# Optimization experiments

Measured on AMD Instinct MI355X. Metric: run time of the kernel, lower is better.

## Reference

```python
import math
import jax, jax.numpy as jnp
import numpy as np

DIM = 512
STYLE_DIM = 512
WS = 8
RES = 64
HEADS = 16
SHIFT = WS // 2
B = 8
EPS = 1e-5


def _rel_pos_index(ws):
    # Faithful replica of the (non-standard) index construction in the source.
    coords = np.stack(np.meshgrid(np.arange(ws), np.arange(ws), indexing='ij')).reshape(2, -1)
    rc = (coords[:, :, None] - coords[:, None, :]).transpose(1, 2, 0).astype(np.int64)
    rc[:, :, 0] += ws - 1
    rc[:, :, 1] += ws - 1
    rc[:, :, 0] += 2 * ws - 1
    return jnp.asarray(rc.sum(-1))  # (ws*ws, ws*ws)


def _attn_mask2(res, ws):
    shift = ws // 2
    m = np.zeros((res, res), dtype=np.float32)
    cnt = 0
    for hs in [slice(0, -ws), slice(-ws, -shift), slice(-shift, None)]:
        for wsl in [slice(0, -ws), slice(-ws, -shift), slice(-shift, None)]:
            m[hs, wsl] = cnt
            cnt += 1
    mw = m.reshape(res // ws, ws, res // ws, ws).transpose(0, 2, 1, 3).reshape(-1, ws * ws)
    am = mw[:, None, :] - mw[:, :, None]  # (nW, N, N)
    return jnp.asarray(np.where(am != 0, -100.0, 0.0).astype(np.float32))


_RPI = _rel_pos_index(WS)
_MASK2 = _attn_mask2(RES, WS)


def _win_part(x, ws):
    Bc, H, W, C = x.shape
    x = x.reshape(Bc, H // ws, ws, W // ws, ws, C).transpose(0, 1, 3, 2, 4, 5)
    return x.reshape(-1, ws * ws, C)


def _win_rev(x, ws, H, W):
    nH, nW = H // ws, W // ws
    C = x.shape[-1]
    x = x.reshape(-1, nH, nW, ws, ws, C).transpose(0, 1, 3, 2, 4, 5)
    return x.reshape(-1, H, W, C)


def _adain(x, style, w, b):
    # x: (B, N, C); InstanceNorm1d over the token dim N per channel (biased var, no affine).
    scale = 1.0 / math.sqrt(w.shape[1])
    s = style @ (w * scale).T + b  # (B, 2C)
    C = x.shape[-1]
    gamma, beta = s[:, :C], s[:, C:]
    mean = x.mean(axis=1, keepdims=True)
    var = x.var(axis=1, keepdims=True)
    xn = (x - mean) / jnp.sqrt(var + EPS)
    return gamma[:, None, :] * xn + beta[:, None, :]


def _window_attn(q, k, v, ws, heads, rpb, rpi, mask):
    # q/k/v: (B, H, W, C)
    C = q.shape[-1]
    hd = C // heads
    qk_scale = hd ** -0.5
    qw = _win_part(q, ws)  # (Bw, N, C)
    kw = _win_part(k, ws)
    vw = _win_part(v, ws)
    Bw, N, _ = qw.shape
    qw = qw.reshape(Bw, N, heads, hd).transpose(0, 2, 1, 3)
    kw = kw.reshape(Bw, N, heads, hd).transpose(0, 2, 1, 3)
    vw = vw.reshape(Bw, N, heads, hd).transpose(0, 2, 1, 3)
    attn = jnp.einsum('bhnd,bhmd->bhnm', qw, kw) * qk_scale
    bias = rpb[rpi.reshape(-1)].reshape(N, N, heads).transpose(2, 0, 1)  # (h, N, N)
    attn = attn + bias[None]
    if mask is not None:
        nW = mask.shape[0]
        attn = attn.reshape(Bw // nW, nW, heads, N, N) + mask[None, :, None]
        attn = attn.reshape(Bw, heads, N, N)
    attn = jax.nn.softmax(attn, axis=-1)
    out = jnp.einsum('bhnm,bhmd->bhnd', attn, vw)
    return out.transpose(0, 2, 1, 3).reshape(Bw, N, C)


def _forward(x, style, ada1_w, ada1_b, qkv_w, qkv_b, rpb1, rpb2,
             proj_w, proj_b, ada2_w, ada2_b, mlp_w1, mlp_b1, mlp_w2, mlp_b2):
    H = W = RES
    Bc, N, C = x.shape
    shortcut = x
    xn = _adain(x, style, ada1_w, ada1_b)
    qkv = xn @ qkv_w.T + qkv_b  # (B, N, 3C)
    qkv = qkv.reshape(Bc, N, 3, C).transpose(2, 0, 1, 3).reshape(3, Bc, H, W, C)
    qkv1 = qkv[..., : C // 2]
    qkv2 = qkv[..., C // 2:]
    qkv2 = jnp.roll(qkv2, shift=(-SHIFT, -SHIFT), axis=(2, 3))
    x1 = _window_attn(qkv1[0], qkv1[1], qkv1[2], WS, HEADS // 2, rpb1, _RPI, None)
    x2 = _window_attn(qkv2[0], qkv2[1], qkv2[2], WS, HEADS // 2, rpb2, _RPI, _MASK2)
    x1 = _win_rev(x1, WS, H, W)
    x2 = _win_rev(x2, WS, H, W)
    x2 = jnp.roll(x2, shift=(SHIFT, SHIFT), axis=(1, 2))
    out = jnp.concatenate([x1, x2], axis=-1).reshape(Bc, N, C)
    out = out @ proj_w.T + proj_b
    out = shortcut + out
    xn2 = _adain(out, style, ada2_w, ada2_b)
    h = xn2 @ mlp_w1.T + mlp_b1
    h = jax.nn.gelu(h, approximate=False)  # erf-based gelu matches source
    h = h @ mlp_w2.T + mlp_b2
    return out + h


def setup_inputs() -> dict:
    key = jax.random.key(0)
    ks = jax.random.split(key, 16)
    rn = lambda k, shp, s: jax.random.normal(k, shp, dtype=jnp.float32) * s
    return {
        'x': rn(ks[0], (B, RES * RES, DIM), 1.0),
        'style': rn(ks[1], (B, STYLE_DIM), 1.0),
        'ada1_w': rn(ks[2], (2 * DIM, STYLE_DIM), 1.0),
        'ada1_b': rn(ks[3], (2 * DIM,), 0.02),
        'qkv_w': rn(ks[4], (3 * DIM, DIM), 0.02),
        'qkv_b': rn(ks[5], (3 * DIM,), 0.02),
        'rpb1': rn(ks[6], ((2 * WS - 1) ** 2, HEADS // 2), 0.02),
        'rpb2': rn(ks[7], ((2 * WS - 1) ** 2, HEADS // 2), 0.02),
        'proj_w': rn(ks[8], (DIM, DIM), 0.02),
        'proj_b': rn(ks[9], (DIM,), 0.02),
        'ada2_w': rn(ks[10], (2 * DIM, STYLE_DIM), 1.0),
        'ada2_b': rn(ks[11], (2 * DIM,), 0.02),
        'mlp_w1': rn(ks[12], (4 * DIM, DIM), 0.02),
        'mlp_b1': rn(ks[13], (4 * DIM,), 0.02),
        'mlp_w2': rn(ks[14], (DIM, 4 * DIM), 0.02),
        'mlp_b2': rn(ks[15], (DIM,), 0.02),
    }


def reference(x, style, ada1_w, ada1_b, qkv_w, qkv_b, rpb1, rpb2,
              proj_w, proj_b, ada2_w, ada2_b, mlp_w1, mlp_b1, mlp_w2, mlp_b2):
    return _forward(x, style, ada1_w, ada1_b, qkv_w, qkv_b, rpb1, rpb2,
                    proj_w, proj_b, ada2_w, ada2_b, mlp_w1, mlp_b1, mlp_w2, mlp_b2)
```

## Files before the change

### kernel.cpp

```cpp
#include <hip/hip_runtime.h>
#include <math.h>

typedef __attribute__((ext_vector_type(8))) short short8;
typedef __attribute__((ext_vector_type(4))) float f32x4;
typedef unsigned short ushort_t;

__device__ __forceinline__ float bf2f(ushort_t u) {
    return __uint_as_float(((unsigned int)u) << 16);
}
__device__ __forceinline__ ushort_t f2bf(float f) {
    unsigned int u = __float_as_uint(f);
    unsigned int r = u + 0x7fffu + ((u >> 16) & 1u);
    return (ushort_t)(r >> 16);
}

__device__ __forceinline__ void async_cp16(const void* g, void* l) {
    __builtin_amdgcn_global_load_lds((const __attribute__((address_space(1))) void*)g,
                                     (__attribute__((address_space(3))) void*)l, 16, 0, 0);
}

__device__ __forceinline__ float fast_gelu(float v) {
    float u2 = 2.0f * v * (0.7978845608028654f + 0.0356774081f * v * v);
    float e = __expf(u2);
    float r = 1.0f / (e + 1.0f);
    return v - v * r;
}

__global__ __launch_bounds__(256) void conv_zero(
        const float* __restrict__ qkv_w, ushort_t* __restrict__ qkv_wb,
        const float* __restrict__ proj_w, ushort_t* __restrict__ proj_wb,
        const float* __restrict__ w1, ushort_t* __restrict__ w1b,
        const float* __restrict__ w2, ushort_t* __restrict__ w2b,
        float* __restrict__ psum2, float* __restrict__ psq2) {
    int i = blockIdx.x * 256 + threadIdx.x;
    if (i < 786432) {
        qkv_wb[i] = f2bf(qkv_w[i]);
    } else if (i < 1048576) {
        int j = i - 786432; proj_wb[j] = f2bf(proj_w[j]);
    } else if (i < 2097152) {
        int j = i - 1048576; w1b[j] = f2bf(w1[j]);
    } else if (i < 3145728) {
        int j = i - 2097152; w2b[j] = f2bf(w2[j]);
    } else {
        int j = i - 3145728;
        psum2[j] = 0.f; psq2[j] = 0.f;
    }
}

__global__ __launch_bounds__(256) void style_kernel(const float* __restrict__ style,
        const float* __restrict__ w1, const float* __restrict__ b1,
        const float* __restrict__ w2, const float* __restrict__ b2,
        float* __restrict__ s1, float* __restrict__ s2) {
    int t = blockIdx.x * 256 + threadIdx.x;
    int which = t >> 13;
    int idx = t & 8191;
    int b = idx >> 10, j = idx & 1023;
    const float* w = which ? w2 : w1;
    const float* bb = which ? b2 : b1;
    const float* st = style + b * 512;
    const float* wr = w + (size_t)j * 512;
    float acc = 0.f;
    for (int k = 0; k < 512; ++k) acc += st[k] * wr[k];
    float v = acc * 0.04419417382415922f + bb[j];
    (which ? s2 : s1)[idx] = v;
}

__global__ __launch_bounds__(512) void stats_part(const float* __restrict__ x,
        float* __restrict__ psum, float* __restrict__ psq) {
    int b = blockIdx.x >> 5;
    int ch = blockIdx.x & 31;
    int c = threadIdx.x;
    const float* p = x + ((size_t)b * 4096 + (size_t)ch * 128) * 512 + c;
    float s = 0.f, q = 0.f;
    for (int t = 0; t < 128; ++t) {
        float v = p[(size_t)t * 512];
        s += v; q += v * v;
    }
    psum[(size_t)blockIdx.x * 512 + c] = s;
    psq [(size_t)blockIdx.x * 512 + c] = q;
}

__global__ __launch_bounds__(256) void stats_fin(const float* __restrict__ psum,
        const float* __restrict__ psq, float* __restrict__ mean, float* __restrict__ rstd) {
    int i = blockIdx.x * 256 + threadIdx.x;
    int b = i >> 9, c = i & 511;
    float s = 0.f, q = 0.f;
    for (int ch = 0; ch < 32; ++ch) {
        s += psum[(size_t)(b * 32 + ch) * 512 + c];
        q += psq [(size_t)(b * 32 + ch) * 512 + c];
    }
    float m = s * (1.f / 4096.f);
    float v = q * (1.f / 4096.f) - m * m;
    mean[i] = m;
    rstd[i] = rsqrtf(v + 1e-5f);
}

__global__ __launch_bounds__(256) void stats_fin2(const float* __restrict__ psum2,
        const float* __restrict__ psq2, float* __restrict__ mean, float* __restrict__ rstd) {
    int i = blockIdx.x * 256 + threadIdx.x;
    float m = psum2[i] * (1.f / 4096.f);
    float v = psq2[i] * (1.f / 4096.f) - m * m;
    mean[i] = m;
    rstd[i] = rsqrtf(v + 1e-5f);
}

__global__ __launch_bounds__(256) void adain_kernel(const float* __restrict__ x,
        const float* __restrict__ s, const float* __restrict__ mean,
        const float* __restrict__ rstd, ushort_t* __restrict__ xn) {
    size_t i4 = (size_t)blockIdx.x * 256 + threadIdx.x;
    size_t e = i4 * 4;
    int b = (int)(e >> 21);
    int c = (int)(e & 511);
    float4 xv = *(const float4*)(x + e);
    float vals[4] = {xv.x, xv.y, xv.z, xv.w};
    ushort_t o[4];
#pragma unroll
    for (int j = 0; j < 4; ++j) {
        int cc = c + j;
        float g  = s[b * 1024 + cc];
        float be = s[b * 1024 + 512 + cc];
        float mn = mean[b * 512 + cc];
        float rs = rstd[b * 512 + cc];
        o[j] = f2bf(g * (vals[j] - mn) * rs + be);
    }
    unsigned long long packed = (unsigned long long)o[0] |
        ((unsigned long long)o[1] << 16) | ((unsigned long long)o[2] << 32) |
        ((unsigned long long)o[3] << 48);
    *(unsigned long long*)(xn + e) = packed;
}

template<int EPI>
__global__ __launch_bounds__(512, 2) void gemm256(
        const ushort_t* __restrict__ A, const ushort_t* __restrict__ Bw,
        const float* __restrict__ bias, const float* __restrict__ resid,
        float* __restrict__ outf, ushort_t* __restrict__ outh,
        float* __restrict__ psum2, float* __restrict__ psq2,
        int N, int K, int gridN, int ntiles, int lnt) {
    __shared__ ushort_t lds[65536];
    const int tid  = threadIdx.x;
    const int lane = tid & 63;
    const int wave = tid >> 6;
    const int wm = wave >> 2, wn = wave & 3;
    const int lm = lane & 15;
    const int kg = lane >> 4;
    const int nt = 1 << lnt;
    const int tpb = ntiles >> 8;

    const int orig = blockIdx.x;
    const int wgid = (orig & 7) * 32 + (orig >> 3);

    unsigned int lo0 = lm * 128 + ((kg * 16) ^ ((lm & 7) << 4));
    unsigned int lo1 = lo0 ^ 64;
    unsigned int vA0 = wm * 16384 + lo0;
    unsigned int vA1 = wm * 16384 + lo1;
    unsigned int vB0 = 65536 + (wn >> 1) * 16384 + (wn & 1) * 8192 + lo0;
    unsigned int vB1 = 65536 + (wn >> 1) * 16384 + (wn & 1) * 8192 + lo1;
    const char* ldsc = (const char*)lds;

    int off[2][2];
#pragma unroll
    for (int rnd = 0; rnd < 2; ++rnd) {
        int chunk = tid + rnd * 512;
        int row = chunk >> 3;
        int g = chunk & 7;
        int gsw = g ^ (row & 7);
#pragma unroll
        for (int h = 0; h < 2; ++h)
            off[h][rnd] = (h * 128 + row) * K + gsw * 8;
    }

    f32x4 acc[8][4];
#pragma unroll
    for (int m = 0; m < 8; ++m)
#pragma unroll
        for (int n = 0; n < 4; ++n)
#pragma unroll
            for (int r = 0; r < 4; ++r) acc[m][n][r] = 0.f;

    auto stage = [&](const ushort_t* __restrict__ mat, long bcur, long bnxt,
                     int dslot, int h, int tt, int isB) {
        long mb = (tt < nt) ? bcur : bnxt;
        int kt = tt & (nt - 1);
        const ushort_t* base = mat + mb + (kt << 6);
        ushort_t* dst = (ushort_t*)lds + isB * 32768 + dslot * 16384 + h * 8192 + tid * 8;
#pragma unroll
        for (int rnd = 0; rnd < 2; ++rnd)
            async_cp16(base + off[h][rnd], dst + rnd * 4096);
    };

    int tcur = wgid;
    int bm = tcur / gridN, bn = tcur - bm * gridN;
    long Am = (long)bm * 256 * K;
    long Bn = (long)bn * 256 * K;

    stage(A,  Am, Am, 0, 0, 0, 0); stage(A,  Am, Am, 0, 1, 0, 0);
    stage(Bw, Bn, Bn, 0, 0, 0, 1); stage(Bw, Bn, Bn, 0, 1, 0, 1);
    stage(Bw, Bn, Bn, 1, 0, 1, 1); stage(Bw, Bn, Bn, 1, 1, 1, 1);
    asm volatile("s_waitcnt vmcnt(4)" ::: "memory");
    __builtin_amdgcn_sched_barrier(0);
    __builtin_amdgcn_s_barrier();

    for (int ti = 0; ti < tpb; ++ti) {
        int tnxt = (ti + 1 < tpb) ? tcur + 256 : tcur;
        int bm2 = tnxt / gridN, bn2 = tnxt - bm2 * gridN;
        long Am2 = (long)bm2 * 256 * K;
        long Bn2 = (long)bn2 * 256 * K;

#pragma unroll 2
        for (int t = 0; t < nt; ++t) {
            const int c = t & 1;
            short8 bfr[4][2];
#pragma unroll
            for (int q = 0; q < 4; ++q) {
                short8 af[2][2];
#pragma unroll
                for (int mq = 0; mq < 2; ++mq) {
                    af[mq][0] = *(const short8*)(ldsc + vA0 + (q * 4096 + mq * 2048));
                    af[mq][1] = *(const short8*)(ldsc + vA1 + (q * 4096 + mq * 2048));
                }
                if (q == 0) {
#pragma unroll
                    for (int n = 0; n < 4; ++n) {
                        bfr[n][0] = *(const short8*)(ldsc + vB0 + n * 2048);
                        bfr[n][1] = *(const short8*)(ldsc + vB1 + n * 2048);
                    }
                }
                if      (q == 0) stage(A,  Am, Am2, c ^ 1, 0, t + 1, 0);
                else if (q == 1) stage(A,  Am, Am2, c ^ 1, 1, t + 1, 0);
                else if (q == 2) stage(Bw, Bn, Bn2, c,     0, t + 2, 1);
                else             stage(Bw, Bn, Bn2, c,     1, t + 2, 1);

                __builtin_amdgcn_s_barrier();
                asm volatile("s_waitcnt lgkmcnt(0)" ::: "memory");
                __builtin_amdgcn_sched_barrier(0);
                __builtin_amdgcn_s_setprio(1);
#pragma unroll
                for (int mq = 0; mq < 2; ++mq)
#pragma unroll
                    for (int n = 0; n < 4; ++n)
#pragma unroll
                        for (int ks = 0; ks < 2; ++ks)
                            acc[q * 2 + mq][n] = __builtin_amdgcn_mfma_f32_16x16x32_bf16(
                                af[mq][ks], bfr[n][ks], acc[q * 2 + mq][n], 0, 0, 0);
                __builtin_amdgcn_s_setprio(0);
                if (q == 3) {
                    asm volatile("s_waitcnt vmcnt(4)" ::: "memory");
                    __builtin_amdgcn_sched_barrier(0);
                }
                __builtin_amdgcn_s_barrier();
            }
            vA0 ^= 32768u; vA1 ^= 32768u; vB0 ^= 32768u; vB1 ^= 32768u;
        }

        const long tile_m = (long)bm * 256;
        const long tile_n = (long)bn * 256;
        float csum[4], csq[4];
        if (EPI == 1) {
#pragma unroll
            for (int n = 0; n < 4; ++n) { csum[n] = 0.f; csq[n] = 0.f; }
        }
#pragma unroll
        for (int m = 0; m < 8; ++m) {
            long row0 = tile_m + wm * 128 + m * 16 + kg * 4;
#pragma unroll
            for (int n = 0; n < 4; ++n) {
                long col = tile_n + wn * 64 + n * 16 + lm;
                float bb = bias[col];
#pragma unroll
                for (int r = 0; r < 4; ++r) {
                    long o = (row0 + r) * (long)N + col;
                    float v = acc[m][n][r] + bb;
                    if (EPI == 0) {
                        outh[o] = f2bf(v);
                    } else if (EPI == 1) {
                        float w = v + resid[o];
                        outf[o] = w;
                        csum[n] += w; csq[n] += w * w;
                    } else if (EPI == 2) {
                        outh[o] = f2bf(fast_gelu(v));
                    } else {
                        outf[o] += v;
                    }
                    acc[m][n][r] = 0.f;
                }
            }
        }
        if (EPI == 1) {
            int b = (int)(tile_m >> 12);
#pragma unroll
            for (int n = 0; n < 4; ++n) {
                int col = (int)(tile_n + wn * 64 + n * 16 + lm);
                atomicAdd(&psum2[b * 512 + col], csum[n]);
                atomicAdd(&psq2 [b * 512 + col], csq[n]);
            }
        }

        tcur = tnxt; bm = bm2; bn = bn2; Am = Am2; Bn = Bn2;
    }
}

__global__ __launch_bounds__(64) void attn_kernel(const ushort_t* __restrict__ qkv,
        const float* __restrict__ rpb1, const float* __restrict__ rpb2,
        ushort_t* __restrict__ attno) {
    __shared__ float klds[64][36];
    __shared__ float vlds[64][36];
    int bid = blockIdx.x;
    int branch = bid >> 12;
    int w_idx  = (bid >> 3) & 511;
    int head   = bid & 7;
    int b = w_idx >> 6, win = w_idx & 63;
    int wh = win >> 3, ww = win & 7;
    int lane = threadIdx.x;
    int ti = lane >> 3, tj = lane & 7;
    int hh = wh * 8 + ti;
    int wp = ww * 8 + tj;
    int hs = branch ? ((hh + 4) & 63) : hh;
    int wsp = branch ? ((wp + 4) & 63) : wp;
    int n = hs * 64 + wsp;
    int c0 = branch * 256 + head * 32;
    const ushort_t* rowp = qkv + (size_t)(b * 4096 + n) * 1536;

    float q[32];
#pragma unroll
    for (int v8 = 0; v8 < 4; ++v8) {
        short8 t = *(const short8*)(rowp + c0 + v8 * 8);
#pragma unroll
        for (int i = 0; i < 8; ++i) q[v8 * 8 + i] = bf2f((ushort_t)t[i]);
    }
#pragma unroll
    for (int v8 = 0; v8 < 4; ++v8) {
        short8 tk = *(const short8*)(rowp + 512  + c0 + v8 * 8);
        short8 tv = *(const short8*)(rowp + 1024 + c0 + v8 * 8);
#pragma unroll
        for (int i = 0; i < 8; ++i) {
            klds[lane][v8 * 8 + i] = bf2f((ushort_t)tk[i]);
            vlds[lane][v8 * 8 + i] = bf2f((ushort_t)tv[i]);
        }
    }
    __syncthreads();

    const float* rpb = branch ? rpb2 : rpb1;
    int code_i = 0;
    if (branch) {
        int gh = (hh < 56) ? 0 : (hh < 60 ? 1 : 2);
        int gw = (wp < 56) ? 0 : (wp < 60 ? 1 : 2);
        code_i = gh * 3 + gw;
    }

    float s[64];
    float mx = -1e30f;
#pragma unroll
    for (int j = 0; j < 64; ++j) {
        int rj = j >> 3, cj = j & 7;
        const float4* kr4 = (const float4*)&klds[j][0];
        float4 k0 = kr4[0], k1 = kr4[1], k2 = kr4[2], k3 = kr4[3];
        float4 k4 = kr4[4], k5 = kr4[5], k6 = kr4[6], k7 = kr4[7];
        float acc =
            q[0]*k0.x + q[1]*k0.y + q[2]*k0.z + q[3]*k0.w +
            q[4]*k1.x + q[5]*k1.y + q[6]*k1.z + q[7]*k1.w +
            q[8]*k2.x + q[9]*k2.y + q[10]*k2.z + q[11]*k2.w +
            q[12]*k3.x + q[13]*k3.y + q[14]*k3.z + q[15]*k3.w +
            q[16]*k4.x + q[17]*k4.y + q[18]*k4.z + q[19]*k4.w +
            q[20]*k5.x + q[21]*k5.y + q[22]*k5.z + q[23]*k5.w +
            q[24]*k6.x + q[25]*k6.y + q[26]*k6.z + q[27]*k6.w +
            q[28]*k7.x + q[29]*k7.y + q[30]*k7.z + q[31]*k7.w;
        float sc = acc * 0.17677669529663687f + rpb[((ti - rj) + (tj - cj) + 29) * 8 + head];
        if (branch) {
            int hj = wh * 8 + rj, wj = ww * 8 + cj;
            int gh = (hj < 56) ? 0 : (hj < 60 ? 1 : 2);
            int gw = (wj < 56) ? 0 : (wj < 60 ? 1 : 2);
            if (gh * 3 + gw != code_i) sc -= 100.f;
        }
        s[j] = sc;
        mx = fmaxf(mx, sc);
    }
    float sum = 0.f;
#pragma unroll
    for (int j = 0; j < 64; ++j) { float e = __expf(s[j] - mx); s[j] = e; sum += e; }
    float inv = 1.f / sum;
    float o[32];
#pragma unroll
    for (int d = 0; d < 32; ++d) o[d] = 0.f;
#pragma unroll
    for (int j = 0; j < 64; ++j) {
        float p = s[j] * inv;
        const float4* vr4 = (const float4*)&vlds[j][0];
#pragma unroll
        for (int d4 = 0; d4 < 8; ++d4) {
            float4 vv = vr4[d4];
            o[d4 * 4 + 0] += p * vv.x;
            o[d4 * 4 + 1] += p * vv.y;
            o[d4 * 4 + 2] += p * vv.z;
            o[d4 * 4 + 3] += p * vv.w;
        }
    }
    ushort_t* op = attno + (size_t)(b * 4096 + n) * 512 + c0;
#pragma unroll
    for (int v8 = 0; v8 < 4; ++v8) {
        short8 t;
#pragma unroll
        for (int i = 0; i < 8; ++i) t[i] = (short)f2bf(o[v8 * 8 + i]);
        *(short8*)(op + v8 * 8) = t;
    }
}

extern "C" void kernel_launch(void* const* d_in, const int* in_sizes, int n_in,
                              void* d_out, int out_size, void* d_ws, size_t ws_size,
                              hipStream_t stream) {
    const float* x      = (const float*)d_in[0];
    const float* style  = (const float*)d_in[1];
    const float* ada1_w = (const float*)d_in[2];
    const float* ada1_b = (const float*)d_in[3];
    const float* qkv_w  = (const float*)d_in[4];
    const float* qkv_b  = (const float*)d_in[5];
    const float* rpb1   = (const float*)d_in[6];
    const float* rpb2   = (const float*)d_in[7];
    const float* proj_w = (const float*)d_in[8];
    const float* proj_b = (const float*)d_in[9];
    const float* ada2_w = (const float*)d_in[10];
    const float* ada2_b = (const float*)d_in[11];
    const float* mlp_w1 = (const float*)d_in[12];
    const float* mlp_b1 = (const float*)d_in[13];
    const float* mlp_w2 = (const float*)d_in[14];
    const float* mlp_b2 = (const float*)d_in[15];
    float* outf = (float*)d_out;

    char* W = (char*)d_ws;
    ushort_t* qkvb    = (ushort_t*)(W);
    ushort_t* attno   = (ushort_t*)(W + 100663296);
    ushort_t* hbuf    = (ushort_t*)(W);
    ushort_t* xn      = (ushort_t*)(W + 134217728);
    ushort_t* qkv_wb  = (ushort_t*)(W + 167772160);
    ushort_t* proj_wb = (ushort_t*)(W + 167772160 + 1572864);
    ushort_t* w1b     = (ushort_t*)(W + 167772160 + 2097152);
    ushort_t* w2b     = (ushort_t*)(W + 167772160 + 4194304);
    float* freg  = (float*)(W + 167772160 + 6291456);
    float* s1    = freg;
    float* s2    = freg + 8192;
    float* mean1 = freg + 16384;
    float* rstd1 = freg + 20480;
    float* mean2 = freg + 24576;
    float* rstd2 = freg + 28672;
    float* psum  = freg + 32768;
    float* psq   = freg + 163840;
    float* psum2 = freg + 294912;
    float* psq2  = freg + 303104;

    conv_zero<<<12320, 256, 0, stream>>>(qkv_w, qkv_wb, proj_w, proj_wb,
                                         mlp_w1, w1b, mlp_w2, w2b, psum2, psq2);

    style_kernel<<<64, 256, 0, stream>>>(style, ada1_w, ada1_b, ada2_w, ada2_b, s1, s2);

    stats_part<<<256, 512, 0, stream>>>(x, psum, psq);
    stats_fin<<<16, 256, 0, stream>>>(psum, psq, mean1, rstd1);
    adain_kernel<<<16384, 256, 0, stream>>>(x, s1, mean1, rstd1, xn);

    gemm256<0><<<256, 512, 0, stream>>>(xn, qkv_wb, qkv_b, nullptr, nullptr, qkvb,
                                        nullptr, nullptr, 1536, 512, 6, 768, 3);

    attn_kernel<<<8192, 64, 0, stream>>>(qkvb, rpb1, rpb2, attno);

    gemm256<1><<<256, 512, 0, stream>>>(attno, proj_wb, proj_b, x, outf, nullptr,
                                        psum2, psq2, 512, 512, 2, 256, 3);

    stats_fin2<<<16, 256, 0, stream>>>(psum2, psq2, mean2, rstd2);
    adain_kernel<<<16384, 256, 0, stream>>>(outf, s2, mean2, rstd2, xn);

    gemm256<2><<<256, 512, 0, stream>>>(xn, w1b, mlp_b1, nullptr, nullptr, hbuf,
                                        nullptr, nullptr, 2048, 512, 8, 1024, 3);
    gemm256<3><<<256, 512, 0, stream>>>(hbuf, w2b, mlp_b2, nullptr, outf, nullptr,
                                        nullptr, nullptr, 512, 2048, 2, 256, 5);
}
```

Baseline: 507.7 us.

## Rewrite window attention with bf16 MFMA and precomputed bias/mask tables

Replaces the scalar fp32 per-thread window attention with a wave-per-(window,head) kernel that computes QK^T and PV using bf16 16x16x32 MFMA instructions, staging V transposed and P in LDS. Relative-position bias and the shifted-window mask are folded into precomputed per-head float tables, built in the existing conversion kernel, so the per-element index and mask logic disappears from the hot loop. Softmax probabilities are rounded to bf16 before the PV product, which adds some precision loss. The tables add a small amount of extra setup work and global reads.

```diff
diff --git a/kernel.cpp b/kernel.cpp
--- a/kernel.cpp
+++ b/kernel.cpp
@@ -4,6 +4,7 @@
 typedef __attribute__((ext_vector_type(8))) short short8;
 typedef __attribute__((ext_vector_type(4))) float f32x4;
 typedef unsigned short ushort_t;
+typedef unsigned long long ull_t;
 
 __device__ __forceinline__ float bf2f(ushort_t u) {
     return __uint_as_float(((unsigned int)u) << 16);
@@ -12,6 +13,11 @@
     unsigned int u = __float_as_uint(f);
     unsigned int r = u + 0x7fffu + ((u >> 16) & 1u);
     return (ushort_t)(r >> 16);
+}
+__device__ __forceinline__ unsigned cvt_pk_bf16(float lo, float hi) {
+    unsigned r;
+    asm volatile("v_cvt_pk_bf16_f32 %0, %1, %2" : "=v"(r) : "v"(lo), "v"(hi));
+    return r;
 }
 
 __device__ __forceinline__ void async_cp16(const void* g, void* l) {
@@ -31,7 +37,9 @@
         const float* __restrict__ proj_w, ushort_t* __restrict__ proj_wb,
         const float* __restrict__ w1, ushort_t* __restrict__ w1b,
         const float* __restrict__ w2, ushort_t* __restrict__ w2b,
-        float* __restrict__ psum2, float* __restrict__ psq2) {
+        float* __restrict__ psum2, float* __restrict__ psq2,
+        const float* __restrict__ rpb1, const float* __restrict__ rpb2,
+        float* __restrict__ tbl0, float* __restrict__ tbl1) {
     int i = blockIdx.x * 256 + threadIdx.x;
     if (i < 786432) {
         qkv_wb[i] = f2bf(qkv_w[i]);
@@ -41,9 +49,31 @@
         int j = i - 1048576; w1b[j] = f2bf(w1[j]);
     } else if (i < 3145728) {
         int j = i - 2097152; w2b[j] = f2bf(w2[j]);
-    } else {
+    } else if (i < 3153920) {
         int j = i - 3145728;
         psum2[j] = 0.f; psq2[j] = 0.f;
+    } else {
+        int t = i - 3153920;
+        if (t < 32768) {
+            int h = t >> 12, ij = t & 4095;
+            int qi = ij >> 6, kj = ij & 63;
+            int idx = ((qi >> 3) - (kj >> 3)) + ((qi & 7) - (kj & 7)) + 29;
+            tbl0[t] = rpb1[idx * 8 + h];
+        } else {
+            int u = t - 32768;
+            int ij = u & 4095;
+            int cls = (u >> 12) & 3;
+            int h = u >> 14;
+            int qi = ij >> 6, kj = ij & 63;
+            int idx = ((qi >> 3) - (kj >> 3)) + ((qi & 7) - (kj & 7)) + 29;
+            float v = rpb2[idx * 8 + h];
+            int gh_i = (cls & 2) ? (((qi >> 3) < 4) ? 1 : 2) : 0;
+            int gw_i = (cls & 1) ? (((qi & 7) < 4) ? 1 : 2) : 0;
+            int gh_j = (cls & 2) ? (((kj >> 3) < 4) ? 1 : 2) : 0;
+            int gw_j = (cls & 1) ? (((kj & 7) < 4) ? 1 : 2) : 0;
+            if (gh_i * 3 + gw_i != gh_j * 3 + gw_j) v -= 100.f;
+            tbl1[u] = v;
+        }
     }
 }
 
@@ -123,10 +153,9 @@
         float rs = rstd[b * 512 + cc];
         o[j] = f2bf(g * (vals[j] - mn) * rs + be);
     }
-    unsigned long long packed = (unsigned long long)o[0] |
-        ((unsigned long long)o[1] << 16) | ((unsigned long long)o[2] << 32) |
-        ((unsigned long long)o[3] << 48);
-    *(unsigned long long*)(xn + e) = packed;
+    ull_t packed = (ull_t)o[0] |
+        ((ull_t)o[1] << 16) | ((ull_t)o[2] << 32) | ((ull_t)o[3] << 48);
+    *(ull_t*)(xn + e) = packed;
 }
 
 template<int EPI>
@@ -299,108 +328,171 @@
     }
 }
 
-__global__ __launch_bounds__(64) void attn_kernel(const ushort_t* __restrict__ qkv,
-        const float* __restrict__ rpb1, const float* __restrict__ rpb2,
+__global__ __launch_bounds__(256) void attn_mfma(const ushort_t* __restrict__ qkv,
+        const float* __restrict__ tbl0, const float* __restrict__ tbl1,
         ushort_t* __restrict__ attno) {
-    __shared__ float klds[64][36];
-    __shared__ float vlds[64][36];
-    int bid = blockIdx.x;
-    int branch = bid >> 12;
-    int w_idx  = (bid >> 3) & 511;
-    int head   = bid & 7;
-    int b = w_idx >> 6, win = w_idx & 63;
-    int wh = win >> 3, ww = win & 7;
-    int lane = threadIdx.x;
-    int ti = lane >> 3, tj = lane & 7;
-    int hh = wh * 8 + ti;
-    int wp = ww * 8 + tj;
-    int hs = branch ? ((hh + 4) & 63) : hh;
-    int wsp = branch ? ((wp + 4) & 63) : wp;
-    int n = hs * 64 + wsp;
-    int c0 = branch * 256 + head * 32;
-    const ushort_t* rowp = qkv + (size_t)(b * 4096 + n) * 1536;
-
-    float q[32];
-#pragma unroll
-    for (int v8 = 0; v8 < 4; ++v8) {
-        short8 t = *(const short8*)(rowp + c0 + v8 * 8);
-#pragma unroll
-        for (int i = 0; i < 8; ++i) q[v8 * 8 + i] = bf2f((ushort_t)t[i]);
-    }
-#pragma unroll
-    for (int v8 = 0; v8 < 4; ++v8) {
-        short8 tk = *(const short8*)(rowp + 512  + c0 + v8 * 8);
-        short8 tv = *(const short8*)(rowp + 1024 + c0 + v8 * 8);
-#pragma unroll
-        for (int i = 0; i < 8; ++i) {
-            klds[lane][v8 * 8 + i] = bf2f((ushort_t)tk[i]);
-            vlds[lane][v8 * 8 + i] = bf2f((ushort_t)tv[i]);
-        }
-    }
-    __syncthreads();
-
-    const float* rpb = branch ? rpb2 : rpb1;
-    int code_i = 0;
-    if (branch) {
-        int gh = (hh < 56) ? 0 : (hh < 60 ? 1 : 2);
-        int gw = (wp < 56) ? 0 : (wp < 60 ? 1 : 2);
-        code_i = gh * 3 + gw;
-    }
-
-    float s[64];
-    float mx = -1e30f;
-#pragma unroll
-    for (int j = 0; j < 64; ++j) {
-        int rj = j >> 3, cj = j & 7;
-        const float4* kr4 = (const float4*)&klds[j][0];
-        float4 k0 = kr4[0], k1 = kr4[1], k2 = kr4[2], k3 = kr4[3];
-        float4 k4 = kr4[4], k5 = kr4[5], k6 = kr4[6], k7 = kr4[7];
-        float acc =
-            q[0]*k0.x + q[1]*k0.y + q[2]*k0.z + q[3]*k0.w +
-            q[4]*k1.x + q[5]*k1.y + q[6]*k1.z + q[7]*k1.w +
-            q[8]*k2.x + q[9]*k2.y + q[10]*k2.z + q[11]*k2.w +
-            q[12]*k3.x + q[13]*k3.y + q[14]*k3.z + q[15]*k3.w +
-            q[16]*k4.x + q[17]*k4.y + q[18]*k4.z + q[19]*k4.w +
-            q[20]*k5.x + q[21]*k5.y + q[22]*k5.z + q[23]*k5.w +
-            q[24]*k6.x + q[25]*k6.y + q[26]*k6.z + q[27]*k6.w +
-            q[28]*k7.x + q[29]*k7.y + q[30]*k7.z + q[31]*k7.w;
-        float sc = acc * 0.17677669529663687f + rpb[((ti - rj) + (tj - cj) + 29) * 8 + head];
-        if (branch) {
-            int hj = wh * 8 + rj, wj = ww * 8 + cj;
-            int gh = (hj < 56) ? 0 : (hj < 60 ? 1 : 2);
-            int gw = (wj < 56) ? 0 : (wj < 60 ? 1 : 2);
-            if (gh * 3 + gw != code_i) sc -= 100.f;
-        }
-        s[j] = sc;
-        mx = fmaxf(mx, sc);
-    }
-    float sum = 0.f;
-#pragma unroll
-    for (int j = 0; j < 64; ++j) { float e = __expf(s[j] - mx); s[j] = e; sum += e; }
-    float inv = 1.f / sum;
-    float o[32];
-#pragma unroll
-    for (int d = 0; d < 32; ++d) o[d] = 0.f;
-#pragma unroll
-    for (int j = 0; j < 64; ++j) {
-        float p = s[j] * inv;
-        const float4* vr4 = (const float4*)&vlds[j][0];
-#pragma unroll
-        for (int d4 = 0; d4 < 8; ++d4) {
-            float4 vv = vr4[d4];
-            o[d4 * 4 + 0] += p * vv.x;
-            o[d4 * 4 + 1] += p * vv.y;
-            o[d4 * 4 + 2] += p * vv.z;
-            o[d4 * 4 + 3] += p * vv.w;
-        }
-    }
-    ushort_t* op = attno + (size_t)(b * 4096 + n) * 512 + c0;
-#pragma unroll
-    for (int v8 = 0; v8 < 4; ++v8) {
-        short8 t;
-#pragma unroll
-        for (int i = 0; i < 8; ++i) t[i] = (short)f2bf(o[v8 * 8 + i]);
-        *(short8*)(op + v8 * 8) = t;
+    __shared__ ushort_t lds[27648];
+    const int tid = threadIdx.x;
+    const int lane = tid & 63;
+    const int wave = tid >> 6;
+    const int job = blockIdx.x * 4 + wave;
+    const int branch = job >> 12;
+    const int w_idx  = (job >> 3) & 511;
+    const int head   = job & 7;
+    const int b = w_idx >> 6, win = w_idx & 63;
+    const int wh = win >> 3, ww = win & 7;
+    const int c0 = branch * 256 + head * 32;
+    const int i_lo = lane & 15;
+    const int kg = lane >> 4;
+
+    ushort_t* Vt = lds + wave * 6912;
+    ushort_t* P  = lds + wave * 6912 + 2304;
+
+    auto tokof = [&](int p) {
+        int hh = wh * 8 + (p >> 3), wp = ww * 8 + (p & 7);
+        if (branch) { hh = (hh + 4) & 63; wp = (wp + 4) & 63; }
+        return b * 4096 + hh * 64 + wp;
+    };
+
+    {
+        const ushort_t* vp = qkv + (size_t)tokof(lane) * 1536 + 1024 + c0;
+        short8 v0 = *(const short8*)(vp);
+        short8 v1 = *(const short8*)(vp + 8);
+        short8 v2 = *(const short8*)(vp + 16);
+        short8 v3 = *(const short8*)(vp + 24);
+#pragma unroll
+        for (int e = 0; e < 8; ++e) {
+            Vt[(e     ) * 72 + lane] = (ushort_t)v0[e];
+            Vt[(e +  8) * 72 + lane] = (ushort_t)v1[e];
+            Vt[(e + 16) * 72 + lane] = (ushort_t)v2[e];
+            Vt[(e + 24) * 72 + lane] = (ushort_t)v3[e];
+        }
+    }
+
+    short8 kf[4], qf[4];
+#pragma unroll
+    for (int m = 0; m < 4; ++m) {
+        size_t rowb = (size_t)tokof(m * 16 + i_lo) * 1536;
+        kf[m] = *(const short8*)(qkv + rowb + 512 + c0 + kg * 8);
+        qf[m] = *(const short8*)(qkv + rowb + c0 + kg * 8);
+    }
+
+    f32x4 s[4][4];
+#pragma unroll
+    for (int mj = 0; mj < 4; ++mj)
+#pragma unroll
+        for (int ni = 0; ni < 4; ++ni)
+#pragma unroll
+            for (int r = 0; r < 4; ++r) s[mj][ni][r] = 0.f;
+#pragma unroll
+    for (int mj = 0; mj < 4; ++mj)
+#pragma unroll
+        for (int ni = 0; ni < 4; ++ni)
+            s[mj][ni] = __builtin_amdgcn_mfma_f32_16x16x32_bf16(kf[mj], qf[ni], s[mj][ni], 0, 0, 0);
+
+    const float* tb;
+    if (branch == 0) {
+        tb = tbl0 + head * 4096;
+    } else {
+        int cls = ((wh == 7) ? 2 : 0) | ((ww == 7) ? 1 : 0);
+        tb = tbl1 + (head * 4 + cls) * 4096;
+    }
+#pragma unroll
+    for (int ni = 0; ni < 4; ++ni) {
+        int i = ni * 16 + i_lo;
+#pragma unroll
+        for (int mj = 0; mj < 4; ++mj) {
+            float4 bv = *(const float4*)(tb + i * 64 + mj * 16 + kg * 4);
+            s[mj][ni][0] = s[mj][ni][0] * 0.17677669529663687f + bv.x;
+            s[mj][ni][1] = s[mj][ni][1] * 0.17677669529663687f + bv.y;
+            s[mj][ni][2] = s[mj][ni][2] * 0.17677669529663687f + bv.z;
+            s[mj][ni][3] = s[mj][ni][3] * 0.17677669529663687f + bv.w;
+        }
+    }
+
+    float mx[4], rs[4];
+#pragma unroll
+    for (int ni = 0; ni < 4; ++ni) {
+        float m = -1e30f;
+#pragma unroll
+        for (int mj = 0; mj < 4; ++mj)
+#pragma unroll
+            for (int r = 0; r < 4; ++r) m = fmaxf(m, s[mj][ni][r]);
+        m = fmaxf(m, __shfl_xor(m, 16));
+        m = fmaxf(m, __shfl_xor(m, 32));
+        mx[ni] = m;
+    }
+#pragma unroll
+    for (int ni = 0; ni < 4; ++ni) {
+        float sum = 0.f;
+#pragma unroll
+        for (int mj = 0; mj < 4; ++mj)
+#pragma unroll
+            for (int r = 0; r < 4; ++r) {
+                float e = __expf(s[mj][ni][r] - mx[ni]);
+                s[mj][ni][r] = e;
+                sum += e;
+            }
+        sum += __shfl_xor(sum, 16);
+        sum += __shfl_xor(sum, 32);
+        rs[ni] = sum;
+    }
+
+#pragma unroll
+    for (int ni = 0; ni < 4; ++ni) {
+        int i = ni * 16 + i_lo;
+#pragma unroll
+        for (int mj = 0; mj < 4; ++mj) {
+            unsigned w0 = cvt_pk_bf16(s[mj][ni][0], s[mj][ni][1]);
+            unsigned w1 = cvt_pk_bf16(s[mj][ni][2], s[mj][ni][3]);
+            ull_t w = (ull_t)w0 | ((ull_t)w1 << 32);
+            *(ull_t*)&P[i * 72 + mj * 16 + kg * 4] = w;
+        }
+    }
+    asm volatile("s_waitcnt lgkmcnt(0)" ::: "memory");
+    __builtin_amdgcn_sched_barrier(0);
+
+    short8 va[2][2];
+    short8 pb[4][2];
+#pragma unroll
+    for (int md = 0; md < 2; ++md)
+#pragma unroll
+        for (int ks = 0; ks < 2; ++ks)
+            va[md][ks] = *(const short8*)&Vt[(md * 16 + i_lo) * 72 + ks * 32 + kg * 8];
+#pragma unroll
+    for (int ni = 0; ni < 4; ++ni)
+#pragma unroll
+        for (int ks = 0; ks < 2; ++ks)
+            pb[ni][ks] = *(const short8*)&P[(ni * 16 + i_lo) * 72 + ks * 32 + kg * 8];
+
+    f32x4 o[2][4];
+#pragma unroll
+    for (int md = 0; md < 2; ++md)
+#pragma unroll
+        for (int ni = 0; ni < 4; ++ni)
+#pragma unroll
+            for (int r = 0; r < 4; ++r) o[md][ni][r] = 0.f;
+#pragma unroll
+    for (int md = 0; md < 2; ++md)
+#pragma unroll
+        for (int ni = 0; ni < 4; ++ni)
+#pragma unroll
+            for (int ks = 0; ks < 2; ++ks)
+                o[md][ni] = __builtin_amdgcn_mfma_f32_16x16x32_bf16(va[md][ks], pb[ni][ks], o[md][ni], 0, 0, 0);
+
+#pragma unroll
+    for (int ni = 0; ni < 4; ++ni) {
+        float inv = 1.f / rs[ni];
+        ushort_t* op = attno + (size_t)tokof(ni * 16 + i_lo) * 512 + c0;
+#pragma unroll
+        for (int md = 0; md < 2; ++md) {
+            ushort_t h0 = f2bf(o[md][ni][0] * inv);
+            ushort_t h1 = f2bf(o[md][ni][1] * inv);
+            ushort_t h2 = f2bf(o[md][ni][2] * inv);
+            ushort_t h3 = f2bf(o[md][ni][3] * inv);
+            ull_t w = (ull_t)h0 | ((ull_t)h1 << 16) | ((ull_t)h2 << 32) | ((ull_t)h3 << 48);
+            *(ull_t*)(op + md * 16 + kg * 4) = w;
+        }
     }
 }
 
@@ -445,9 +537,12 @@
     float* psq   = freg + 163840;
     float* psum2 = freg + 294912;
     float* psq2  = freg + 303104;
-
-    conv_zero<<<12320, 256, 0, stream>>>(qkv_w, qkv_wb, proj_w, proj_wb,
-                                         mlp_w1, w1b, mlp_w2, w2b, psum2, psq2);
+    float* tbl0  = freg + 311296;
+    float* tbl1  = freg + 344064;
+
+    conv_zero<<<12960, 256, 0, stream>>>(qkv_w, qkv_wb, proj_w, proj_wb,
+                                         mlp_w1, w1b, mlp_w2, w2b, psum2, psq2,
+                                         rpb1, rpb2, tbl0, tbl1);
 
     style_kernel<<<64, 256, 0, stream>>>(style, ada1_w, ada1_b, ada2_w, ada2_b, s1, s2);
 
@@ -458,7 +553,7 @@
     gemm256<0><<<256, 512, 0, stream>>>(xn, qkv_wb, qkv_b, nullptr, nullptr, qkvb,
                                         nullptr, nullptr, 1536, 512, 6, 768, 3);
 
-    attn_kernel<<<8192, 64, 0, stream>>>(qkvb, rpb1, rpb2, attno);
+    attn_mfma<<<2048, 256, 0, stream>>>(qkvb, tbl0, tbl1, attno);
 
     gemm256<1><<<256, 512, 0, stream>>>(attno, proj_wb, proj_b, x, outf, nullptr,
                                         psum2, psq2, 512, 512, 2, 256, 3);
```

Result: faster. 443.1 us (-12.7%).
